# Kernel tuning notes

Measured on AMD Instinct MI355X. Metric: run time of the kernel, lower is better.

Reference implementation:

```python
import jax, jax.numpy as jnp
import numpy as np

N = 100000   # nodes
E = 1600000  # edges
D = 128      # input_dim
H = 128      # hidden_dim
G = 64       # graphs in batch
L = 3        # num GCN layers
BN_EPS = 1e-5


def setup_inputs() -> dict:
    key = jax.random.key(0)
    ks = jax.random.split(key, 16)
    s = 1.0 / np.sqrt(H)
    inp = {
        "x": jax.random.normal(ks[0], (N, D), jnp.float32),
        "edge_index": jax.random.randint(ks[1], (2, E), 0, N, dtype=jnp.int64),
        "batch": jnp.sort(jax.random.randint(ks[2], (N,), 0, G, dtype=jnp.int64)),
        # stacked GCNConv params (input_dim == hidden_dim so layer 0 stacks too)
        "conv_w": jax.random.normal(ks[3], (L, H, H), jnp.float32) * s,
        "conv_b": jax.random.normal(ks[4], (L, H), jnp.float32) * 0.01,
        # BatchNorm1d running stats + affine (eval mode)
        "bn_gamma": jnp.ones((L, H), jnp.float32),
        "bn_beta": jnp.zeros((L, H), jnp.float32),
        "bn_mean": jax.random.normal(ks[5], (L, H), jnp.float32) * 0.1,
        "bn_var": jax.random.uniform(ks[6], (L, H), jnp.float32, 0.5, 1.5),
        # node head MLP
        "node_w1": jax.random.normal(ks[7], (H // 2, H), jnp.float32) * s,
        "node_b1": jnp.zeros((H // 2,), jnp.float32),
        "node_w2": jax.random.normal(ks[8], (2, H // 2), jnp.float32) * (1.0 / np.sqrt(H // 2)),
        "node_b2": jnp.zeros((2,), jnp.float32),
        # graph head MLP
        "graph_w1": jax.random.normal(ks[9], (H // 2, H), jnp.float32) * s,
        "graph_b1": jnp.zeros((H // 2,), jnp.float32),
        "graph_w2": jax.random.normal(ks[10], (2, H // 2), jnp.float32) * (1.0 / np.sqrt(H // 2)),
        "graph_b2": jnp.zeros((2,), jnp.float32),
    }
    return inp


def _gcn_layer(h, src, dst, deg_inv_sqrt, w, b):
    # PyG GCNConv: h' = W h, then symmetric-normalized scatter-add over
    # edges (self-loops already appended to src/dst).
    h = h @ w.T                                   # [N, H]
    norm = deg_inv_sqrt[src] * deg_inv_sqrt[dst]  # [E+N]
    msg = h[src] * norm[:, None]                  # [E+N, H] gather
    out = jax.ops.segment_sum(msg, dst, num_segments=N)  # scatter-add
    return out + b


def _forward(x, edge_index, batch, conv_w, conv_b, bn_gamma, bn_beta,
             bn_mean, bn_var, node_w1, node_b1, node_w2, node_b2,
             graph_w1, graph_b1, graph_w2, graph_b2):
    loops = jnp.arange(N, dtype=edge_index.dtype)
    src = jnp.concatenate([edge_index[0], loops])
    dst = jnp.concatenate([edge_index[1], loops])
    deg = jax.ops.segment_sum(jnp.ones_like(src, dtype=x.dtype), dst,
                              num_segments=N)
    deg_inv_sqrt = jnp.where(deg > 0, jax.lax.rsqrt(deg), 0.0)

    h = x
    for i in range(L):  # conv -> BN(eval) -> ReLU (dropout inactive in eval)
        h = _gcn_layer(h, src, dst, deg_inv_sqrt, conv_w[i], conv_b[i])
        h = (h - bn_mean[i]) * jax.lax.rsqrt(bn_var[i] + BN_EPS) * bn_gamma[i] + bn_beta[i]
        h = jax.nn.relu(h)

    node_pred = jax.nn.relu(h @ node_w1.T + node_b1) @ node_w2.T + node_b2

    counts = jax.ops.segment_sum(jnp.ones((N,), h.dtype), batch,
                                 num_segments=G)
    graph_emb = jax.ops.segment_sum(h, batch, num_segments=G) / \
        jnp.maximum(counts, 1.0)[:, None]
    graph_pred = jax.nn.relu(graph_emb @ graph_w1.T + graph_b1) @ graph_w2.T + graph_b2
    return node_pred, graph_pred


def reference(x, edge_index, batch, conv_w, conv_b, bn_gamma, bn_beta,
              bn_mean, bn_var, node_w1, node_b1, node_w2, node_b2,
              graph_w1, graph_b1, graph_w2, graph_b2):
    return _forward(x, edge_index, batch, conv_w, conv_b, bn_gamma, bn_beta,
                    bn_mean, bn_var, node_w1, node_b1, node_w2, node_b2,
                    graph_w1, graph_b1, graph_w2, graph_b2)
```

## Files before the change

kernel.cpp:

```cpp
#include <hip/hip_runtime.h>
#include <hip/hip_bf16.h>

#define NN 100000
#define EE 1600000
#define HH 128
#define GG 64
#define LL 3
#define BN_EPS 1e-5f
#define NT 391
#define CHW 392
#define CAP 6144

typedef __hip_bfloat16 bf16;
typedef __attribute__((ext_vector_type(8))) short short8;
typedef __attribute__((ext_vector_type(4))) float floatx4;

__device__ __forceinline__ float lo16(unsigned v) { return __uint_as_float(v << 16); }
__device__ __forceinline__ float hi16(unsigned v) { return __uint_as_float(v & 0xffff0000u); }
__device__ __forceinline__ unsigned short f2b(float v) {
    bf16 h = __float2bfloat16(v);
    return *(unsigned short*)&h;
}
__device__ __forceinline__ unsigned pack2(float a, float b) {
    return (unsigned)f2b(a) | ((unsigned)f2b(b) << 16);
}
__device__ __forceinline__ int geti(const int* __restrict__ p, int i, int f) {
    return f ? p[2 * i] : p[i];
}

__global__ __launch_bounds__(1024) void k_part(const int* __restrict__ ei,
        unsigned* __restrict__ chunk, unsigned short* __restrict__ lbu,
        int* __restrict__ flag,
        const float* __restrict__ conv_w, const float* __restrict__ nw1,
        unsigned short* __restrict__ cwB, unsigned short* __restrict__ n1B,
        float* __restrict__ bnA, float* __restrict__ bnB,
        const float* __restrict__ conv_b, const float* __restrict__ g,
        const float* __restrict__ be, const float* __restrict__ mn,
        const float* __restrict__ vr, float* __restrict__ gsum,
        float* __restrict__ gcnt, unsigned* __restrict__ tbz) {
    __shared__ int lcnt[NT];
    __shared__ int sd[512];
    __shared__ unsigned short lbs[CHW];
    __shared__ unsigned sorted[4096];
    int t = threadIdx.x;
    int e0 = blockIdx.x * 4096;
    int probe = ei[2 * (e0 + (t & 63)) + 1];
    int f = __any(probe != 0) ? 0 : 1;
    if (blockIdx.x == 0 && t == 0) *flag = f;
    int gi = blockIdx.x * 1024 + t;
    if (gi < LL * HH * HH) cwB[gi] = f2b(conv_w[gi]);
    if (gi < 64 * HH) n1B[gi] = f2b(nw1[gi]);
    if (gi < LL * HH) {
        float A = g[gi] * rsqrtf(vr[gi] + BN_EPS);
        bnA[gi] = A;
        bnB[gi] = (conv_b[gi] - mn[gi]) * A + be[gi];
    }
    if (gi < GG * HH) gsum[gi] = 0.f;
    if (gi < GG) gcnt[gi] = 0.f;
    if (gi < 64) tbz[(size_t)NN * 64 + gi] = 0u;
    int nume = EE - e0 < 4096 ? EE - e0 : 4096;
    for (int i = t; i < NT; i += 1024) lcnt[i] = 0;
    __syncthreads();
    unsigned pk[4]; int ml[4], mt[4];
#pragma unroll
    for (int i = 0; i < 4; i++) {
        int li = i * 1024 + t;
        if (li < nume) {
            int e = e0 + li;
            int src = geti(ei, e, f), dst = geti(ei, EE + e, f);
            mt[i] = dst >> 8;
            pk[i] = ((unsigned)src << 8) | (unsigned)(dst & 255);
            ml[i] = atomicAdd(&lcnt[mt[i]], 1);
        }
    }
    __syncthreads();
    int own = 0;
    if (t < 512) {
        own = t < NT ? lcnt[t] : 0;
        sd[t] = own;
    }
    __syncthreads();
    for (int off = 1; off < 512; off <<= 1) {
        int y = 0;
        if (t < 512 && t >= off) y = sd[t - off];
        __syncthreads();
        if (t < 512) sd[t] += y;
        __syncthreads();
    }
    if (t < NT) lbs[t] = (unsigned short)(sd[t] - own);
    if (t == 0) lbs[NT] = (unsigned short)nume;
    __syncthreads();
#pragma unroll
    for (int i = 0; i < 4; i++) {
        int li = i * 1024 + t;
        if (li < nume) sorted[(int)lbs[mt[i]] + ml[i]] = pk[i];
    }
    if (t < CHW) lbu[blockIdx.x * CHW + t] = lbs[t];
    __syncthreads();
    for (int idx = t; idx < nume; idx += 1024)
        __builtin_nontemporal_store(sorted[idx], &chunk[e0 + idx]);
}

__global__ __launch_bounds__(1024) void k_csr(const unsigned* __restrict__ chunk,
        const unsigned short* __restrict__ lbu, unsigned* __restrict__ csr,
        int* __restrict__ offs, int* __restrict__ cnt, float* __restrict__ dinv) {
    __shared__ unsigned stage[CAP];
    __shared__ unsigned outb[CAP];
    __shared__ int sd[512];
    __shared__ int hist[256], exs[256], cur[256];
    __shared__ int s_nep;
    int T = blockIdx.x, t = threadIdx.x;
    int st = 0, rl = 0;
    if (t < NT) {
        int s0 = lbu[t * CHW + T];
        int s1 = lbu[t * CHW + T + 1];
        st = t * 4096 + s0;
        rl = s1 - s0;
    }
    if (t < 512) sd[t] = rl;
    __syncthreads();
    for (int off = 1; off < 512; off <<= 1) {
        int y = 0;
        if (t < 512 && t >= off) y = sd[t - off];
        __syncthreads();
        if (t < 512) sd[t] += y;
        __syncthreads();
    }
    int ne = sd[511];
    if (ne > CAP) ne = CAP;
    int so = t < NT ? sd[t] - rl : 0;
    if (t < 256) hist[t] = 0;
    __syncthreads();
    if (t < NT) {
        for (int j = 0; j < rl; j++) {
            int p = so + j;
            if (p < CAP)
                stage[p] = __builtin_nontemporal_load(&chunk[st + j]);
        }
    }
    __syncthreads();
    for (int i = t; i < ne; i += 1024)
        atomicAdd(&hist[stage[i] & 255u], 1);
    __syncthreads();
    int c = 0, pc = 0;
    if (t < 256) {
        c = hist[t];
        pc = (c + 7) & ~7;
        exs[t] = pc;
    }
    __syncthreads();
    for (int off = 1; off < 256; off <<= 1) {
        int a = 0;
        if (t < 256 && t >= off) a = exs[t - off];
        __syncthreads();
        if (t < 256) exs[t] += a;
        __syncthreads();
    }
    if (t < 256) {
        int stn = exs[t] - pc;
        cur[t] = stn;
        int node = T * 256 + t;
        if (node < NN) {
            offs[node] = T * CAP + stn;
            cnt[node] = c;
            dinv[node] = rsqrtf(1.0f + (float)c);
        }
        for (int i = stn + c; i < stn + pc && i < CAP; i++)
            outb[i] = NN;
        if (t == 255) s_nep = exs[255] < CAP ? exs[255] : CAP;
    }
    __syncthreads();
    for (int i = t; i < ne; i += 1024) {
        unsigned p = stage[i];
        int q = atomicAdd(&cur[p & 255u], 1);
        if (q < CAP) outb[q] = p >> 8;
    }
    __syncthreads();
    int nep = s_nep;
    for (int i = t; i < nep; i += 1024)
        csr[(size_t)T * CAP + i] = outb[i];
}

template<typename AT, int NC, bool FUSE>
__global__ __launch_bounds__(256) void k_gemm(const AT* __restrict__ in,
        const unsigned short* __restrict__ Wb, const float* __restrict__ bias,
        unsigned short* __restrict__ outh, int do_relu,
        const float* __restrict__ scale,
        const float* __restrict__ w2, const float* __restrict__ b2v,
        float* __restrict__ out2f) {
    __shared__ char sB[NC * 272];
    int wave = threadIdx.x >> 6, lane = threadIdx.x & 63;
    int ln = lane & 15, q = lane >> 4;
    {
        const short8* wsrc = (const short8*)Wb;
        for (int i = threadIdx.x; i < NC * 16; i += 256) {
            short8 v = wsrc[i];
            *(short8*)(sB + (i >> 4) * 272 + (i & 15) * 16) = v;
        }
    }
    int r0 = blockIdx.x * 64 + wave * 16;
    int row = r0 + ln;
    int rr = row < NN ? row : NN - 1;
    short8 a[4];
    if constexpr (sizeof(AT) == 2) {
        const short8* ap = (const short8*)(in + (size_t)rr * HH);
#pragma unroll
        for (int kt = 0; kt < 4; kt++) a[kt] = ap[kt * 4 + q];
    } else {
        const float4* ap = (const float4*)(in + (size_t)rr * HH);
#pragma unroll
        for (int kt = 0; kt < 4; kt++) {
            float4 f0 = ap[(kt * 4 + q) * 2];
            float4 f1 = ap[(kt * 4 + q) * 2 + 1];
            a[kt][0] = (short)f2b(f0.x); a[kt][1] = (short)f2b(f0.y);
            a[kt][2] = (short)f2b(f0.z); a[kt][3] = (short)f2b(f0.w);
            a[kt][4] = (short)f2b(f1.x); a[kt][5] = (short)f2b(f1.y);
            a[kt][6] = (short)f2b(f1.z); a[kt][7] = (short)f2b(f1.w);
        }
    }
    float scl[4];
    if constexpr (!FUSE) {
#pragma unroll
        for (int reg = 0; reg < 4; reg++) {
            int orow = r0 + q * 4 + reg;
            scl[reg] = scale ? scale[orow < NN ? orow : NN - 1] : 1.f;
        }
    }
    __syncthreads();
    float p0[4], p1[4];
    if constexpr (FUSE) {
#pragma unroll
        for (int r = 0; r < 4; r++) { p0[r] = 0.f; p1[r] = 0.f; }
    }
#pragma unroll
    for (int ct = 0; ct < NC / 16; ct++) {
        int c = ct * 16 + ln;
        floatx4 acc = {0.f, 0.f, 0.f, 0.f};
#pragma unroll
        for (int kt = 0; kt < 4; kt++) {
            short8 b = *(const short8*)(sB + (size_t)c * 272 + kt * 64 + q * 16);
            acc = __builtin_amdgcn_mfma_f32_16x16x32_bf16(a[kt], b, acc, 0, 0, 0);
        }
        float bv = bias ? bias[c] : 0.f;
        if constexpr (FUSE) {
            float wa = w2[c], wb = w2[64 + c];
#pragma unroll
            for (int reg = 0; reg < 4; reg++) {
                float v = fmaxf(acc[reg] + bv, 0.f);
                p0[reg] = fmaf(v, wa, p0[reg]);
                p1[reg] = fmaf(v, wb, p1[reg]);
            }
        } else {
#pragma unroll
            for (int reg = 0; reg < 4; reg++) {
                int orow = r0 + q * 4 + reg;
                if (orow < NN) {
                    float v = acc[reg] + bv;
                    if (do_relu) v = fmaxf(v, 0.f);
                    outh[(size_t)orow * NC + c] = f2b(v * scl[reg]);
                }
            }
        }
    }
    if constexpr (FUSE) {
#pragma unroll
        for (int off = 1; off < 16; off <<= 1) {
#pragma unroll
            for (int r = 0; r < 4; r++) {
                p0[r] += __shfl_xor(p0[r], off);
                p1[r] += __shfl_xor(p1[r], off);
            }
        }
        if (ln == 0) {
            float ba = b2v[0], bb = b2v[1];
#pragma unroll
            for (int reg = 0; reg < 4; reg++) {
                int orow = r0 + q * 4 + reg;
                if (orow < NN)
                    ((float2*)out2f)[orow] = make_float2(p0[reg] + ba, p1[reg] + bb);
            }
        }
    }
}

__global__ __launch_bounds__(256) void k_aggr(const unsigned* __restrict__ tbs,
        const unsigned* __restrict__ csr, const int* __restrict__ offs,
        const int* __restrict__ cnt, const float* __restrict__ dinv,
        const float* __restrict__ bnA, const float* __restrict__ bnB,
        unsigned* __restrict__ hout) {
    int wave = threadIdx.x >> 6, lane = threadIdx.x & 63;
    int node = blockIdx.x * 4 + wave;
    if (node >= NN) return;
    int base = __builtin_amdgcn_readfirstlane(offs[node]);
    int ne   = __builtin_amdgcn_readfirstlane(cnt[node]);
    float dd = __uint_as_float(__builtin_amdgcn_readfirstlane(
                   (int)__float_as_uint(dinv[node])));
    unsigned sv = tbs[(size_t)node * 64 + lane];
    float ax = lo16(sv), ay = hi16(sv);
    const unsigned* __restrict__ ep = csr + base;
    int nr = (ne + 7) & ~7;
    for (int k0 = 0; k0 < nr; k0 += 8) {
        unsigned vv[8];
#pragma unroll
        for (int j = 0; j < 8; j++) {
            int s = (int)ep[k0 + j];
            const unsigned* rp = tbs + (size_t)s * 64;
            vv[j] = rp[lane];
        }
#pragma unroll
        for (int j = 0; j < 8; j++) {
            ax += lo16(vv[j]);
            ay += hi16(vv[j]);
        }
    }
    float2 A = ((const float2*)bnA)[lane];
    float2 B = ((const float2*)bnB)[lane];
    float r0 = fmaxf(fmaf(ax * dd, A.x, B.x), 0.f);
    float r1 = fmaxf(fmaf(ay * dd, A.y, B.y), 0.f);
    __builtin_nontemporal_store(pack2(r0, r1), &hout[(size_t)node * 64 + lane]);
}

#define PN 32
__global__ __launch_bounds__(64) void k_pool(const unsigned* __restrict__ hb,
        const int* __restrict__ batch, float* __restrict__ gsum,
        float* __restrict__ gcnt, const int* __restrict__ flag) {
    int lane = threadIdx.x;
    int f = *flag;
    int s0 = blockIdx.x * PN;
    int cur = geti(batch, s0, f);
    float a0 = 0.f, a1 = 0.f, cn = 0.f;
    auto step = [&](int g, unsigned v) {
        if (g != cur) {
            atomicAdd(&gsum[cur * HH + 2 * lane], a0);
            atomicAdd(&gsum[cur * HH + 2 * lane + 1], a1);
            if (lane == 0) atomicAdd(&gcnt[cur], cn);
            a0 = a1 = cn = 0.f; cur = g;
        }
        a0 += lo16(v); a1 += hi16(v); cn += 1.f;
    };
    for (int n = s0; n < s0 + PN; n += 4) {
        int g0 = geti(batch, n, f),     g1 = geti(batch, n + 1, f);
        int g2 = geti(batch, n + 2, f), g3 = geti(batch, n + 3, f);
        unsigned v0 = hb[(size_t)n * 64 + lane];
        unsigned v1 = hb[(size_t)(n + 1) * 64 + lane];
        unsigned v2 = hb[(size_t)(n + 2) * 64 + lane];
        unsigned v3 = hb[(size_t)(n + 3) * 64 + lane];
        step(g0, v0); step(g1, v1); step(g2, v2); step(g3, v3);
    }
    atomicAdd(&gsum[cur * HH + 2 * lane], a0);
    atomicAdd(&gsum[cur * HH + 2 * lane + 1], a1);
    if (lane == 0) atomicAdd(&gcnt[cur], cn);
}

__global__ __launch_bounds__(64) void k_ghead(const float* __restrict__ gsum,
        const float* __restrict__ gcnt, const float* __restrict__ w1,
        const float* __restrict__ b1, const float* __restrict__ w2,
        const float* __restrict__ b2v, float* __restrict__ out) {
    __shared__ float emb[HH];
    int g = blockIdx.x, lane = threadIdx.x;
    float cn = gcnt[g];
    cn = cn > 1.f ? cn : 1.f;
    float inv = 1.f / cn;
    emb[lane] = gsum[g * HH + lane] * inv;
    emb[lane + 64] = gsum[g * HH + 64 + lane] * inv;
    __syncthreads();
    float acc = b1[lane];
    for (int k = 0; k < HH; k++) acc = fmaf(emb[k], w1[lane * HH + k], acc);
    float y = fmaxf(acc, 0.f);
    float v0 = y * w2[lane];
    float v1 = y * w2[64 + lane];
#pragma unroll
    for (int off = 32; off; off >>= 1) {
        v0 += __shfl_xor(v0, off);
        v1 += __shfl_xor(v1, off);
    }
    if (lane == 0) {
        out[(size_t)NN * 2 + g * 2]     = v0 + b2v[0];
        out[(size_t)NN * 2 + g * 2 + 1] = v1 + b2v[1];
    }
}

extern "C" void kernel_launch(void* const* d_in, const int* in_sizes, int n_in,
                              void* d_out, int out_size, void* d_ws, size_t ws_size,
                              hipStream_t stream) {
    const float* x      = (const float*)d_in[0];
    const int*   ei     = (const int*)d_in[1];
    const int*   batch  = (const int*)d_in[2];
    const float* conv_w = (const float*)d_in[3];
    const float* conv_b = (const float*)d_in[4];
    const float* bn_g   = (const float*)d_in[5];
    const float* bn_b   = (const float*)d_in[6];
    const float* bn_m   = (const float*)d_in[7];
    const float* bn_v   = (const float*)d_in[8];
    const float* nw1    = (const float*)d_in[9];
    const float* nb1    = (const float*)d_in[10];
    const float* nw2    = (const float*)d_in[11];
    const float* nb2    = (const float*)d_in[12];
    const float* gw1    = (const float*)d_in[13];
    const float* gb1    = (const float*)d_in[14];
    const float* gw2    = (const float*)d_in[15];
    const float* gb2    = (const float*)d_in[16];
    float* out = (float*)d_out;

    char* ws = (char*)d_ws;
    size_t off = 0;
    auto alloc = [&](size_t bytes) -> void* {
        void* p = ws + off;
        off += (bytes + 255) & ~(size_t)255;
        return p;
    };
    unsigned short* hb   = (unsigned short*)alloc((size_t)NN * HH * 2);
    unsigned short* tb   = (unsigned short*)alloc((size_t)(NN + 1) * HH * 2);
    unsigned* chunk  = (unsigned*)alloc((size_t)EE * 4);
    unsigned* csr    = (unsigned*)alloc((size_t)NT * CAP * 4);
    unsigned short* lbu = (unsigned short*)alloc((size_t)NT * CHW * 2);
    int*      offs   = (int*)     alloc((size_t)NN * 4);
    int*      cnt    = (int*)     alloc((size_t)NN * 4);
    float*    dinv   = (float*)   alloc((size_t)NN * 4);
    float*    bnA    = (float*)   alloc((size_t)LL * HH * 4);
    float*    bnB    = (float*)   alloc((size_t)LL * HH * 4);
    float*    gsum   = (float*)   alloc((size_t)GG * HH * 4);
    float*    gcnt   = (float*)   alloc((size_t)GG * 4);
    unsigned short* cwB = (unsigned short*)alloc((size_t)LL * HH * HH * 2);
    unsigned short* n1B = (unsigned short*)alloc((size_t)64 * HH * 2);
    int*      flag   = (int*)     alloc(256);

    k_part<<<NT, 1024, 0, stream>>>(ei, chunk, lbu, flag, conv_w, nw1, cwB, n1B,
            bnA, bnB, conv_b, bn_g, bn_b, bn_m, bn_v, gsum, gcnt, (unsigned*)tb);
    k_csr<<<NT, 1024, 0, stream>>>(chunk, lbu, csr, offs, cnt, dinv);

    k_gemm<float, HH, false><<<(NN + 63) / 64, 256, 0, stream>>>(
        x, cwB, nullptr, tb, 0, dinv, nullptr, nullptr, nullptr);
    k_aggr<<<(NN + 3) / 4, 256, 0, stream>>>((const unsigned*)tb, csr, offs, cnt,
                                             dinv, bnA, bnB, (unsigned*)hb);
    for (int l = 1; l < LL; l++) {
        k_gemm<unsigned short, HH, false><<<(NN + 63) / 64, 256, 0, stream>>>(
            hb, cwB + (size_t)l * HH * HH, nullptr, tb, 0, dinv,
            nullptr, nullptr, nullptr);
        k_aggr<<<(NN + 3) / 4, 256, 0, stream>>>((const unsigned*)tb, csr, offs,
                                                 cnt, dinv, bnA + l * HH,
                                                 bnB + l * HH, (unsigned*)hb);
    }

    k_gemm<unsigned short, 64, true><<<(NN + 63) / 64, 256, 0, stream>>>(
        hb, n1B, nb1, nullptr, 1, nullptr, nw2, nb2, out);

    k_pool<<<(NN + PN - 1) / PN, 64, 0, stream>>>((const unsigned*)hb, batch,
                                                  gsum, gcnt, flag);
    k_ghead<<<GG, 64, 0, stream>>>(gsum, gcnt, gw1, gb1, gw2, gb2, out);
}
```

Before: 437.9 us.

## Slice feature buffers into 16-column planes and aggregate 8 nodes per wave

Stores the bf16 node-feature buffers as 8 column slices of 16 features (32 bytes per node per slice). Each aggregation block now handles one slice for 32 nodes, so the gathered working set per launch is smaller and stays cache-resident. Within a wave, 8 nodes are processed at once, with edge indices shared via ds_bpermute. CSR rows are padded to the max degree of each group of 8 nodes, so every lane group in a wave runs the same trip count. The GEMM, pool and head kernels are adapted to the sliced layout. The cost is extra padded edges for high-degree groups and a larger CAP, which raises LDS use.

```diff
diff --git a/kernel.cpp b/kernel.cpp
--- a/kernel.cpp
+++ b/kernel.cpp
@@ -9,7 +9,8 @@
 #define BN_EPS 1e-5f
 #define NT 391
 #define CHW 392
-#define CAP 6144
+#define CAP 7680
+#define SLS (NN + 1)
 
 typedef __hip_bfloat16 bf16;
 typedef __attribute__((ext_vector_type(8))) short short8;
@@ -57,7 +58,10 @@
     }
     if (gi < GG * HH) gsum[gi] = 0.f;
     if (gi < GG) gcnt[gi] = 0.f;
-    if (gi < 64) tbz[(size_t)NN * 64 + gi] = 0u;
+    if (gi < 64) {
+        int s = gi >> 3, cc = gi & 7;
+        tbz[(size_t)s * (SLS * 8) + (size_t)NN * 8 + cc] = 0u;
+    }
     int nume = EE - e0 < 4096 ? EE - e0 : 4096;
     for (int i = t; i < NT; i += 1024) lcnt[i] = 0;
     __syncthreads();
@@ -103,11 +107,12 @@
 
 __global__ __launch_bounds__(1024) void k_csr(const unsigned* __restrict__ chunk,
         const unsigned short* __restrict__ lbu, unsigned* __restrict__ csr,
-        int* __restrict__ offs, int* __restrict__ cnt, float* __restrict__ dinv) {
+        int* __restrict__ offs, int* __restrict__ gnr, float* __restrict__ dinv) {
     __shared__ unsigned stage[CAP];
     __shared__ unsigned outb[CAP];
     __shared__ int sd[512];
-    __shared__ int hist[256], exs[256], cur[256];
+    __shared__ int hist[256], cur[256];
+    __shared__ int gmax[32], gexs[32];
     __shared__ int s_nep;
     int T = blockIdx.x, t = threadIdx.x;
     int st = 0, rl = 0;
@@ -130,6 +135,7 @@
     if (ne > CAP) ne = CAP;
     int so = t < NT ? sd[t] - rl : 0;
     if (t < 256) hist[t] = 0;
+    if (t < 32) gmax[t] = 0;
     __syncthreads();
     if (t < NT) {
         for (int j = 0; j < rl; j++) {
@@ -142,33 +148,31 @@
     for (int i = t; i < ne; i += 1024)
         atomicAdd(&hist[stage[i] & 255u], 1);
     __syncthreads();
-    int c = 0, pc = 0;
+    int c = 0;
     if (t < 256) {
         c = hist[t];
-        pc = (c + 7) & ~7;
-        exs[t] = pc;
-    }
-    __syncthreads();
-    for (int off = 1; off < 256; off <<= 1) {
-        int a = 0;
-        if (t < 256 && t >= off) a = exs[t - off];
-        __syncthreads();
-        if (t < 256) exs[t] += a;
-        __syncthreads();
-    }
+        atomicMax(&gmax[t >> 3], (c + 7) & ~7);
+    }
+    __syncthreads();
+    if (t == 0) {
+        int run = 0;
+        for (int i = 0; i < 32; i++) { gexs[i] = run; run += 8 * gmax[i]; }
+        s_nep = run < CAP ? run : CAP;
+    }
+    __syncthreads();
     if (t < 256) {
-        int stn = exs[t] - pc;
+        int gm = gmax[t >> 3];
+        int stn = gexs[t >> 3] + (t & 7) * gm;
         cur[t] = stn;
         int node = T * 256 + t;
         if (node < NN) {
             offs[node] = T * CAP + stn;
-            cnt[node] = c;
             dinv[node] = rsqrtf(1.0f + (float)c);
         }
-        for (int i = stn + c; i < stn + pc && i < CAP; i++)
+        for (int i = stn + c; i < stn + gm && i < CAP; i++)
             outb[i] = NN;
-        if (t == 255) s_nep = exs[255] < CAP ? exs[255] : CAP;
-    }
+    }
+    if (t < 32) gnr[T * 32 + t] = gmax[t];
     __syncthreads();
     for (int i = t; i < ne; i += 1024) {
         unsigned p = stage[i];
@@ -203,9 +207,13 @@
     int rr = row < NN ? row : NN - 1;
     short8 a[4];
     if constexpr (sizeof(AT) == 2) {
-        const short8* ap = (const short8*)(in + (size_t)rr * HH);
-#pragma unroll
-        for (int kt = 0; kt < 4; kt++) a[kt] = ap[kt * 4 + q];
+        const unsigned short* sp = (const unsigned short*)in;
+#pragma unroll
+        for (int kt = 0; kt < 4; kt++) {
+            int i = kt * 4 + q;
+            a[kt] = *(const short8*)(sp + (size_t)(i >> 1) * ((size_t)SLS * 16)
+                                        + (size_t)rr * 16 + (i & 1) * 8);
+        }
     } else {
         const float4* ap = (const float4*)(in + (size_t)rr * HH);
 #pragma unroll
@@ -257,7 +265,8 @@
                 if (orow < NN) {
                     float v = acc[reg] + bv;
                     if (do_relu) v = fmaxf(v, 0.f);
-                    outh[(size_t)orow * NC + c] = f2b(v * scl[reg]);
+                    outh[(size_t)ct * ((size_t)SLS * 16) + (size_t)orow * 16 + ln]
+                        = f2b(v * scl[reg]);
                 }
             }
         }
@@ -285,39 +294,45 @@
 
 __global__ __launch_bounds__(256) void k_aggr(const unsigned* __restrict__ tbs,
         const unsigned* __restrict__ csr, const int* __restrict__ offs,
-        const int* __restrict__ cnt, const float* __restrict__ dinv,
+        const int* __restrict__ gnr, const float* __restrict__ dinv,
         const float* __restrict__ bnA, const float* __restrict__ bnB,
         unsigned* __restrict__ hout) {
+    int slice = blockIdx.x & 7, chunk = blockIdx.x >> 3;
     int wave = threadIdx.x >> 6, lane = threadIdx.x & 63;
-    int node = blockIdx.x * 4 + wave;
-    if (node >= NN) return;
-    int base = __builtin_amdgcn_readfirstlane(offs[node]);
-    int ne   = __builtin_amdgcn_readfirstlane(cnt[node]);
-    float dd = __uint_as_float(__builtin_amdgcn_readfirstlane(
-                   (int)__float_as_uint(dinv[node])));
-    unsigned sv = tbs[(size_t)node * 64 + lane];
+    int c = lane & 7;
+    int node = chunk * 32 + wave * 8 + (lane >> 3);
+    const char* __restrict__ ts = (const char*)(tbs + (size_t)slice * (SLS * 8));
+    int base = offs[node];
+    int gm = gnr[chunk * 4 + wave];
+    float dd = dinv[node];
+    unsigned sv = *(const unsigned*)(ts + ((unsigned)node * 32u + (unsigned)c * 4u));
     float ax = lo16(sv), ay = hi16(sv);
-    const unsigned* __restrict__ ep = csr + base;
-    int nr = (ne + 7) & ~7;
-    for (int k0 = 0; k0 < nr; k0 += 8) {
+    int bp = (lane & 56) << 2;
+    unsigned eo = (unsigned)(base + c) * 4u;
+    unsigned m = __builtin_nontemporal_load(
+        (const unsigned*)((const char*)csr + eo));
+    for (int k0 = 0; k0 < gm; k0 += 8) {
+        unsigned mn = __builtin_nontemporal_load(
+            (const unsigned*)((const char*)csr + eo + (unsigned)(k0 + 8) * 4u));
         unsigned vv[8];
 #pragma unroll
         for (int j = 0; j < 8; j++) {
-            int s = (int)ep[k0 + j];
-            const unsigned* rp = tbs + (size_t)s * 64;
-            vv[j] = rp[lane];
+            unsigned e = (unsigned)__builtin_amdgcn_ds_bpermute(bp + j * 4, (int)m);
+            vv[j] = *(const unsigned*)(ts + (e * 32u + (unsigned)c * 4u));
         }
 #pragma unroll
         for (int j = 0; j < 8; j++) {
             ax += lo16(vv[j]);
             ay += hi16(vv[j]);
         }
-    }
-    float2 A = ((const float2*)bnA)[lane];
-    float2 B = ((const float2*)bnB)[lane];
+        m = mn;
+    }
+    float2 A = ((const float2*)bnA)[slice * 8 + c];
+    float2 B = ((const float2*)bnB)[slice * 8 + c];
     float r0 = fmaxf(fmaf(ax * dd, A.x, B.x), 0.f);
     float r1 = fmaxf(fmaf(ay * dd, A.y, B.y), 0.f);
-    __builtin_nontemporal_store(pack2(r0, r1), &hout[(size_t)node * 64 + lane]);
+    __builtin_nontemporal_store(pack2(r0, r1),
+        &hout[(size_t)slice * (SLS * 8) + (size_t)node * 8 + c]);
 }
 
 #define PN 32
@@ -328,6 +343,7 @@
     int f = *flag;
     int s0 = blockIdx.x * PN;
     int cur = geti(batch, s0, f);
+    size_t sb = (size_t)(lane >> 3) * (SLS * 8) + (lane & 7);
     float a0 = 0.f, a1 = 0.f, cn = 0.f;
     auto step = [&](int g, unsigned v) {
         if (g != cur) {
@@ -338,14 +354,15 @@
         }
         a0 += lo16(v); a1 += hi16(v); cn += 1.f;
     };
-    for (int n = s0; n < s0 + PN; n += 4) {
-        int g0 = geti(batch, n, f),     g1 = geti(batch, n + 1, f);
-        int g2 = geti(batch, n + 2, f), g3 = geti(batch, n + 3, f);
-        unsigned v0 = hb[(size_t)n * 64 + lane];
-        unsigned v1 = hb[(size_t)(n + 1) * 64 + lane];
-        unsigned v2 = hb[(size_t)(n + 2) * 64 + lane];
-        unsigned v3 = hb[(size_t)(n + 3) * 64 + lane];
-        step(g0, v0); step(g1, v1); step(g2, v2); step(g3, v3);
+    for (int n = s0; n < s0 + PN; n += 8) {
+        int gg[8]; unsigned vv[8];
+#pragma unroll
+        for (int j = 0; j < 8; j++) {
+            gg[j] = geti(batch, n + j, f);
+            vv[j] = hb[sb + (size_t)(n + j) * 8];
+        }
+#pragma unroll
+        for (int j = 0; j < 8; j++) step(gg[j], vv[j]);
     }
     atomicAdd(&gsum[cur * HH + 2 * lane], a0);
     atomicAdd(&gsum[cur * HH + 2 * lane + 1], a1);
@@ -409,13 +426,13 @@
         off += (bytes + 255) & ~(size_t)255;
         return p;
     };
-    unsigned short* hb   = (unsigned short*)alloc((size_t)NN * HH * 2);
-    unsigned short* tb   = (unsigned short*)alloc((size_t)(NN + 1) * HH * 2);
+    unsigned* hb     = (unsigned*)alloc((size_t)SLS * 256);
+    unsigned* tb     = (unsigned*)alloc((size_t)SLS * 256);
     unsigned* chunk  = (unsigned*)alloc((size_t)EE * 4);
-    unsigned* csr    = (unsigned*)alloc((size_t)NT * CAP * 4);
+    unsigned* csr    = (unsigned*)alloc((size_t)NT * CAP * 4 + 256);
     unsigned short* lbu = (unsigned short*)alloc((size_t)NT * CHW * 2);
     int*      offs   = (int*)     alloc((size_t)NN * 4);
-    int*      cnt    = (int*)     alloc((size_t)NN * 4);
+    int*      gnr    = (int*)     alloc((size_t)NT * 32 * 4);
     float*    dinv   = (float*)   alloc((size_t)NN * 4);
     float*    bnA    = (float*)   alloc((size_t)LL * HH * 4);
     float*    bnB    = (float*)   alloc((size_t)LL * HH * 4);
@@ -426,26 +443,25 @@
     int*      flag   = (int*)     alloc(256);
 
     k_part<<<NT, 1024, 0, stream>>>(ei, chunk, lbu, flag, conv_w, nw1, cwB, n1B,
-            bnA, bnB, conv_b, bn_g, bn_b, bn_m, bn_v, gsum, gcnt, (unsigned*)tb);
-    k_csr<<<NT, 1024, 0, stream>>>(chunk, lbu, csr, offs, cnt, dinv);
+            bnA, bnB, conv_b, bn_g, bn_b, bn_m, bn_v, gsum, gcnt, tb);
+    k_csr<<<NT, 1024, 0, stream>>>(chunk, lbu, csr, offs, gnr, dinv);
 
     k_gemm<float, HH, false><<<(NN + 63) / 64, 256, 0, stream>>>(
-        x, cwB, nullptr, tb, 0, dinv, nullptr, nullptr, nullptr);
-    k_aggr<<<(NN + 3) / 4, 256, 0, stream>>>((const unsigned*)tb, csr, offs, cnt,
-                                             dinv, bnA, bnB, (unsigned*)hb);
+        x, cwB, nullptr, (unsigned short*)tb, 0, dinv, nullptr, nullptr, nullptr);
+    k_aggr<<<8 * (NN / 32), 256, 0, stream>>>(tb, csr, offs, gnr,
+                                              dinv, bnA, bnB, hb);
     for (int l = 1; l < LL; l++) {
         k_gemm<unsigned short, HH, false><<<(NN + 63) / 64, 256, 0, stream>>>(
-            hb, cwB + (size_t)l * HH * HH, nullptr, tb, 0, dinv,
-            nullptr, nullptr, nullptr);
-        k_aggr<<<(NN + 3) / 4, 256, 0, stream>>>((const unsigned*)tb, csr, offs,
-                                                 cnt, dinv, bnA + l * HH,
-                                                 bnB + l * HH, (unsigned*)hb);
+            (const unsigned short*)hb, cwB + (size_t)l * HH * HH, nullptr,
+            (unsigned short*)tb, 0, dinv, nullptr, nullptr, nullptr);
+        k_aggr<<<8 * (NN / 32), 256, 0, stream>>>(tb, csr, offs, gnr,
+                                                  dinv, bnA + l * HH,
+                                                  bnB + l * HH, hb);
     }
 
     k_gemm<unsigned short, 64, true><<<(NN + 63) / 64, 256, 0, stream>>>(
-        hb, n1B, nb1, nullptr, 1, nullptr, nw2, nb2, out);
-
-    k_pool<<<(NN + PN - 1) / PN, 64, 0, stream>>>((const unsigned*)hb, batch,
-                                                  gsum, gcnt, flag);
+        (const unsigned short*)hb, n1B, nb1, nullptr, 1, nullptr, nw2, nb2, out);
+
+    k_pool<<<(NN + PN - 1) / PN, 64, 0, stream>>>(hb, batch, gsum, gcnt, flag);
     k_ghead<<<GG, 64, 0, stream>>>(gsum, gcnt, gw1, gb1, gw2, gb2, out);
 }
```

Result: slower. 633.8 us (+44.7%).
